# Optimization experiments

Measured on AMD Instinct MI355X. Metric: run time of the kernel, lower is better.

The kernel has to match this reference:

```python
import math
import jax, jax.numpy as jnp
import numpy as np

B, N, D, E, DN, H, M = 32, 64, 256, 32, 64, 8, 32
EPS = 1e-5


def _ln(x):
    # param-free layer norm over the last axis
    mu = jnp.mean(x, axis=-1, keepdims=True)
    var = jnp.var(x, axis=-1, keepdims=True)
    return (x - mu) * jax.lax.rsqrt(var + EPS)


def setup_inputs() -> dict:
    key = jax.random.key(0)
    ks = jax.random.split(key, 9)
    embeddings = jax.random.normal(ks[0], (B, N, D), dtype=jnp.float32)
    edge_features = jax.random.normal(ks[1], (B, N, N, E), dtype=jnp.float32)
    mask = jax.random.randint(ks[2], (B, N), 0, 2).astype(bool)
    node_features = jax.random.normal(ks[3], (B, N, DN), dtype=jnp.float32)
    s = lambda d: 1.0 / math.sqrt(d)
    W_edge = jax.random.normal(ks[4], (E, H, M), dtype=jnp.float32) * s(E)
    W_recv = jax.random.normal(ks[5], (D, H, M), dtype=jnp.float32) * s(D)
    W_send = jax.random.normal(ks[6], (D, H, M), dtype=jnp.float32) * s(D)
    W_recv_node = jax.random.normal(ks[7], (DN, H, M), dtype=jnp.float32) * s(DN)
    W_send_node = jax.random.normal(ks[8], (DN, H, M), dtype=jnp.float32) * s(DN)
    return dict(embeddings=embeddings, edge_features=edge_features, mask=mask,
                node_features=node_features, W_edge=W_edge, W_recv=W_recv,
                W_send=W_send, W_recv_node=W_recv_node, W_send_node=W_send_node)


def reference(embeddings, edge_features, mask, node_features,
              W_edge, W_recv, W_send, W_recv_node, W_send_node):
    sqrt2 = math.sqrt(2.0)
    mask_f = mask.astype(embeddings.dtype)  # [B, N]
    emb = _ln(embeddings) * mask_f[..., None]  # [B, N, D]
    # double mask: [B, sender, receiver, 1]
    dm = (mask_f[..., None, :, None] * mask_f[..., :, None, None])
    ef = edge_features * dm  # [B, N, N, E]
    # projections to (heads, message_dim)
    edge_part = jnp.einsum('bije,ehm->bijhm', ef, W_edge)        # [B,N,N,H,M]
    recv = jnp.einsum('bjd,dhm->bjhm', emb, W_recv) / sqrt2      # [B,N,H,M]
    send = jnp.einsum('bid,dhm->bihm', emb, W_send) / sqrt2
    # receiver broadcast over sender axis (-4), sender over receiver axis (-3)
    rs = jnp.tanh(recv[..., None, :, :, :] + send[..., :, None, :, :])  # [B,N,N,H,M]
    rn = jnp.einsum('bjd,dhm->bjhm', node_features, W_recv_node)
    sn = jnp.einsum('bid,dhm->bihm', node_features, W_send_node)
    rs = rs * jax.nn.sigmoid((rn[..., None, :, :, :] + sn[..., :, None, :, :]) / sqrt2)
    msgs = rs * edge_part * dm[..., None]  # [B,N,N,H,M]
    updates = msgs.sum(axis=-4)            # sum over senders -> [B,N,H,M]
    updates = _ln(updates)
    return jnp.reshape(updates, (*updates.shape[:-2], -1))  # [B,N,H*M]
```

## Files before the change

kernel.cpp:

```cpp
#include <hip/hip_runtime.h>
#include <hip/hip_bf16.h>
#include <math.h>

#define B_   32
#define N_   64
#define D_   256
#define E_   32
#define DN_  64
#define H_   8
#define M_   32
#define HM_  256
#define BN_  2048
#define EPS_ 1e-5f
#define INV_SQRT2 0.70710678118654752f

typedef float f32x4 __attribute__((ext_vector_type(4)));
typedef short bf16x8 __attribute__((ext_vector_type(8)));
union U4S8 { uint4 u; bf16x8 s; };

__device__ __forceinline__ unsigned pk2(float a, float b) {
    union { __hip_bfloat162 h; unsigned u; } cv;
    cv.h = __float22bfloat162_rn(make_float2(a, b));
    return cv.u;
}


__global__ __launch_bounds__(256, 1) void node_k(
        const float* __restrict__ emb, const float* __restrict__ nfeat,
        const int* __restrict__ mraw,
        const float* __restrict__ Wr, const float* __restrict__ Ws,
        const float* __restrict__ Wrn, const float* __restrict__ Wsn,
        float2* __restrict__ g_rr, float2* __restrict__ g_ssC,
        int* __restrict__ cnt, int* __restrict__ sidx,
        unsigned long long* __restrict__ mask64) {
    const int t = threadIdx.x;
    const int w = t >> 6, l = t & 63, hi = l >> 4, lo = l & 15;
    const int b = blockIdx.x >> 1, half = blockIdx.x & 1;
    const int nbase = half * 128 + w * 32;

    __shared__ int s_flag, cnt_sh;
    __shared__ float mfb[N_];
    __shared__ int sidx_s[N_], pos_s[N_];
    __shared__ __align__(16) unsigned short eln[64 * 256];
    __shared__ __align__(16) unsigned short nfs[64 * 64];

    if (t == 0) s_flag = 0;
    __syncthreads();
    {
        int v0 = mraw[t], v1 = mraw[t + 256];
        if (((v0 | v1) & ~1) != 0) atomicOr(&s_flag, 1);
    }
    __syncthreads();
    const bool bytef = (s_flag != 0);
    if (t < N_) {
        const unsigned char* mb = (const unsigned char*)mraw;
        const int k = b * N_ + t;
        mfb[t] = bytef ? (mb[k] ? 1.0f : 0.0f) : (mraw[k] ? 1.0f : 0.0f);
    }
    __syncthreads();
    if (t == 0) {
        int c = 0; unsigned long long bits = 0;
        for (int i = 0; i < N_; ++i) {
            if (mfb[i] > 0.5f) { bits |= (1ull << i); sidx_s[c] = i; pos_s[i] = c; ++c; }
            else pos_s[i] = -1;
        }
        cnt_sh = c;
        for (int p = c; p < N_; ++p) sidx_s[p] = -1;
        if (half == 0) { cnt[b] = c; mask64[b] = bits; }
    }
    __syncthreads();
    if (half == 0 && t < N_) sidx[b * N_ + t] = sidx_s[t];

    for (int rr = 0; rr < 16; ++rr) {
        const int i = w * 16 + rr;
        float4 x = *(const float4*)(emb + (size_t)(b * N_ + i) * D_ + l * 4);
        float s  = x.x + x.y + x.z + x.w;
        float s2 = x.x*x.x + x.y*x.y + x.z*x.z + x.w*x.w;
        #pragma unroll
        for (int k = 32; k >= 1; k >>= 1) { s += __shfl_xor(s, k); s2 += __shfl_xor(s2, k); }
        float mu  = s * (1.0f / D_);
        float var = s2 * (1.0f / D_) - mu * mu;
        float rs  = rsqrtf(var + EPS_) * mfb[i];
        unsigned p0 = pk2((x.x - mu) * rs, (x.y - mu) * rs);
        unsigned p1 = pk2((x.z - mu) * rs, (x.w - mu) * rs);
        unsigned off = (unsigned)(i * 512) + (((unsigned)(l * 8)) ^ (((unsigned)(i & 15)) << 4));
        *(uint2*)((char*)eln + off) = make_uint2(p0, p1);
    }
    #pragma unroll
    for (int it = 0; it < 4; ++it) {
        const int idx = it * 1024 + t * 4;
        const int r = idx >> 6, c = idx & 63;
        float4 x = *(const float4*)(nfeat + (size_t)(b * N_ + r) * DN_ + c);
        unsigned p0 = pk2(x.x, x.y), p1 = pk2(x.z, x.w);
        unsigned off = (unsigned)(r * 128) + (((unsigned)(c * 2)) ^ (((unsigned)(r & 7)) << 4));
        *(uint2*)((char*)nfs + off) = make_uint2(p0, p1);
    }
    __syncthreads();

    f32x4 aR[4][2], aS[4][2], aRN[4][2], aSN[4][2];
    #pragma unroll
    for (int mt = 0; mt < 4; ++mt)
        #pragma unroll
        for (int nt = 0; nt < 2; ++nt) {
            aR[mt][nt] = (f32x4){0,0,0,0}; aS[mt][nt] = (f32x4){0,0,0,0};
            aRN[mt][nt] = (f32x4){0,0,0,0}; aSN[mt][nt] = (f32x4){0,0,0,0};
        }

    for (int ks = 0; ks < 8; ++ks) {
        U4S8 af[4];
        #pragma unroll
        for (int mt = 0; mt < 4; ++mt) {
            const int i = mt * 16 + lo;
            unsigned o = (unsigned)(ks * 64 + hi * 16);
            af[mt].u = *(const uint4*)((const char*)eln +
                          (unsigned)(i * 512) + (o ^ (((unsigned)(i & 15)) << 4)));
        }
        U4S8 br[2], bs[2];
        #pragma unroll
        for (int nt = 0; nt < 2; ++nt) {
            const int n = nbase + nt * 16 + lo;
            const float* wr = Wr + (size_t)(ks * 32 + hi * 8) * HM_ + n;
            const float* ws = Ws + (size_t)(ks * 32 + hi * 8) * HM_ + n;
            float r0=wr[0*HM_], r1=wr[1*HM_], r2=wr[2*HM_], r3=wr[3*HM_];
            float r4=wr[4*HM_], r5=wr[5*HM_], r6=wr[6*HM_], r7=wr[7*HM_];
            br[nt].u = make_uint4(pk2(r0,r1), pk2(r2,r3), pk2(r4,r5), pk2(r6,r7));
            float s0=ws[0*HM_], s1=ws[1*HM_], s2=ws[2*HM_], s3=ws[3*HM_];
            float s4=ws[4*HM_], s5=ws[5*HM_], s6=ws[6*HM_], s7=ws[7*HM_];
            bs[nt].u = make_uint4(pk2(s0,s1), pk2(s2,s3), pk2(s4,s5), pk2(s6,s7));
        }
        #pragma unroll
        for (int mt = 0; mt < 4; ++mt)
            #pragma unroll
            for (int nt = 0; nt < 2; ++nt) {
                aR[mt][nt] = __builtin_amdgcn_mfma_f32_16x16x32_bf16(af[mt].s, br[nt].s, aR[mt][nt], 0, 0, 0);
                aS[mt][nt] = __builtin_amdgcn_mfma_f32_16x16x32_bf16(af[mt].s, bs[nt].s, aS[mt][nt], 0, 0, 0);
            }
        if (ks < 2) {
            U4S8 a2[4];
            #pragma unroll
            for (int mt = 0; mt < 4; ++mt) {
                const int i = mt * 16 + lo;
                unsigned o = (unsigned)(ks * 64 + hi * 16);
                a2[mt].u = *(const uint4*)((const char*)nfs +
                              (unsigned)(i * 128) + (o ^ (((unsigned)(i & 7)) << 4)));
            }
            U4S8 brn[2], bsn[2];
            #pragma unroll
            for (int nt = 0; nt < 2; ++nt) {
                const int n = nbase + nt * 16 + lo;
                const float* wr = Wrn + (size_t)(ks * 32 + hi * 8) * HM_ + n;
                const float* ws = Wsn + (size_t)(ks * 32 + hi * 8) * HM_ + n;
                float r0=wr[0*HM_], r1=wr[1*HM_], r2=wr[2*HM_], r3=wr[3*HM_];
                float r4=wr[4*HM_], r5=wr[5*HM_], r6=wr[6*HM_], r7=wr[7*HM_];
                brn[nt].u = make_uint4(pk2(r0,r1), pk2(r2,r3), pk2(r4,r5), pk2(r6,r7));
                float s0=ws[0*HM_], s1=ws[1*HM_], s2=ws[2*HM_], s3=ws[3*HM_];
                float s4=ws[4*HM_], s5=ws[5*HM_], s6=ws[6*HM_], s7=ws[7*HM_];
                bsn[nt].u = make_uint4(pk2(s0,s1), pk2(s2,s3), pk2(s4,s5), pk2(s6,s7));
            }
            #pragma unroll
            for (int mt = 0; mt < 4; ++mt)
                #pragma unroll
                for (int nt = 0; nt < 2; ++nt) {
                    aRN[mt][nt] = __builtin_amdgcn_mfma_f32_16x16x32_bf16(a2[mt].s, brn[nt].s, aRN[mt][nt], 0, 0, 0);
                    aSN[mt][nt] = __builtin_amdgcn_mfma_f32_16x16x32_bf16(a2[mt].s, bsn[nt].s, aSN[mt][nt], 0, 0, 0);
                }
        }
    }

    const int cb = cnt_sh;
    #pragma unroll
    for (int mt = 0; mt < 4; ++mt) {
        #pragma unroll
        for (int r = 0; r < 4; ++r) {
            const int i = mt * 16 + hi * 4 + r;
            const int p = pos_s[i];
            #pragma unroll
            for (int nt = 0; nt < 2; ++nt) {
                const int n = nbase + nt * 16 + lo;
                g_rr[(size_t)(b * N_ + i) * HM_ + n] =
                    make_float2(aR[mt][nt][r] * INV_SQRT2, aRN[mt][nt][r] * INV_SQRT2);
                if (p >= 0)
                    g_ssC[(size_t)(b * N_ + p) * HM_ + n] =
                        make_float2(aS[mt][nt][r] * INV_SQRT2, aSN[mt][nt][r] * INV_SQRT2);
            }
        }
    }
    for (int pp = cb + w; pp < N_; pp += 4) {
        float4 z = {0, 0, 0, 0};
        *(float4*)&g_ssC[(size_t)(b * N_ + pp) * HM_ + half * 128 + l * 2] = z;
    }
}

__global__ __launch_bounds__(256) void edge_agg(
        const float* __restrict__ edge,
        const unsigned long long* __restrict__ mask64,
        const int* __restrict__ cnt, const int* __restrict__ sidx,
        const float* __restrict__ We,
        const float2* __restrict__ g_rr, const float2* __restrict__ g_ssC,
        float* __restrict__ out) {
    const int t  = threadIdx.x;
    const int bn = blockIdx.x;
    const int b  = bn >> 6;
    const int j  = bn & 63;
    const int w  = t >> 6, l = t & 63, hi = l >> 4, lo = l & 15;

    if (!((mask64[b] >> j) & 1ull)) {
        out[bn * HM_ + t] = 0.0f;
        return;
    }
    const int cb = cnt[b];

    __shared__ uint4 ldsA[256];
    {
        const int mt = t >> 6, phi = (t >> 4) & 3, plo = t & 15;
        const int si = sidx[b * N_ + mt * 16 + plo];
        uint4 u = make_uint4(0, 0, 0, 0);
        if (si >= 0) {
            const float* src = edge + ((size_t)((b * N_ + si) * N_ + j)) * E_ + phi * 8;
            float4 v0 = *(const float4*)src;
            float4 v1 = *(const float4*)(src + 4);
            u = make_uint4(pk2(v0.x, v0.y), pk2(v0.z, v0.w),
                           pk2(v1.x, v1.y), pk2(v1.z, v1.w));
        }
        ldsA[t] = u;
    }
    __syncthreads();

    U4S8 b4[4];
    #pragma unroll
    for (int nl = 0; nl < 4; ++nl) {
        const int n = w * 64 + nl * 16 + lo;
        const float* wp = We + (size_t)(hi * 8) * HM_ + n;
        float w0=wp[0*HM_], w1=wp[1*HM_], w2=wp[2*HM_], w3=wp[3*HM_];
        float w4=wp[4*HM_], w5=wp[5*HM_], w6=wp[6*HM_], w7=wp[7*HM_];
        b4[nl].u = make_uint4(pk2(w0,w1), pk2(w2,w3), pk2(w4,w5), pk2(w6,w7));
    }

    float2 rr[4];
    #pragma unroll
    for (int nl = 0; nl < 4; ++nl) rr[nl] = g_rr[bn * HM_ + w * 64 + nl * 16 + lo];

    const f32x4 zero = {0.0f, 0.0f, 0.0f, 0.0f};
    float upd[4] = {0.0f, 0.0f, 0.0f, 0.0f};

    #pragma unroll
    for (int mt = 0; mt < 4; ++mt) {
        if (mt * 16 < cb) {
            U4S8 a4; a4.u = ldsA[mt * 64 + l];
            f32x4 acc[4];
            #pragma unroll
            for (int nl = 0; nl < 4; ++nl)
                acc[nl] = __builtin_amdgcn_mfma_f32_16x16x32_bf16(a4.s, b4[nl].s, zero, 0, 0, 0);

            #pragma unroll
            for (int r = 0; r < 4; ++r) {
                const int p = mt * 16 + hi * 4 + r;
                const float2* ssrow = g_ssC + (size_t)(b * N_ + p) * HM_;
                #pragma unroll
                for (int nl = 0; nl < 4; ++nl) {
                    float2 ss = ssrow[w * 64 + nl * 16 + lo];
                    float ep = acc[nl][r];
                    float tx = rr[nl].x + ss.x;
                    float E1 = __expf(2.0f * tx);
                    float th = fmaf(-2.0f, __builtin_amdgcn_rcpf(E1 + 1.0f), 1.0f);
                    float z  = rr[nl].y + ss.y;
                    float sg = __builtin_amdgcn_rcpf(1.0f + __expf(-z));
                    upd[nl] = fmaf(th * sg, ep, upd[nl]);
                }
            }
        }
    }

    #pragma unroll
    for (int nl = 0; nl < 4; ++nl) {
        upd[nl] += __shfl_xor(upd[nl], 16);
        upd[nl] += __shfl_xor(upd[nl], 32);
    }

    float s0 = upd[0] + upd[1], q0 = upd[0]*upd[0] + upd[1]*upd[1];
    float s1 = upd[2] + upd[3], q1 = upd[2]*upd[2] + upd[3]*upd[3];
    #pragma unroll
    for (int k = 8; k >= 1; k >>= 1) {
        s0 += __shfl_xor(s0, k); q0 += __shfl_xor(q0, k);
        s1 += __shfl_xor(s1, k); q1 += __shfl_xor(q1, k);
    }
    float mu0 = s0 * (1.0f / M_), va0 = q0 * (1.0f / M_) - mu0 * mu0;
    float mu1 = s1 * (1.0f / M_), va1 = q1 * (1.0f / M_) - mu1 * mu1;
    float rs0 = rsqrtf(va0 + EPS_), rs1 = rsqrtf(va1 + EPS_);
    float val = upd[hi];
    float o = (hi < 2) ? (val - mu0) * rs0 : (val - mu1) * rs1;
    out[bn * HM_ + w * 64 + l] = o;
}

extern "C" void kernel_launch(void* const* d_in, const int* in_sizes, int n_in,
                              void* d_out, int out_size, void* d_ws, size_t ws_size,
                              hipStream_t stream) {
    const float* embeddings = (const float*)d_in[0];
    const float* edge_feat  = (const float*)d_in[1];
    const int*   mask_raw   = (const int*)d_in[2];
    const float* node_feat  = (const float*)d_in[3];
    const float* W_edge     = (const float*)d_in[4];
    const float* W_recv     = (const float*)d_in[5];
    const float* W_send     = (const float*)d_in[6];
    const float* W_recvn    = (const float*)d_in[7];
    const float* W_sendn    = (const float*)d_in[8];
    float* out = (float*)d_out;

    float2* g_ssC = (float2*)d_ws;
    float2* g_rr  = g_ssC + (size_t)BN_ * HM_;
    unsigned long long* mask64 = (unsigned long long*)(g_rr + (size_t)BN_ * HM_);
    int* cnt  = (int*)(mask64 + B_);
    int* sidx = cnt + B_;

    node_k<<<2 * B_, 256, 0, stream>>>(embeddings, node_feat, mask_raw,
                                       W_recv, W_send, W_recvn, W_sendn,
                                       g_rr, g_ssC, cnt, sidx, mask64);
    edge_agg<<<BN_, 256, 0, stream>>>(edge_feat, mask64, cnt, sidx, W_edge,
                                      g_rr, g_ssC, out);
}
```

Before: 42.69 us.

## Fuse node projection and edge aggregation into one cooperative kernel with grid syncs

Replaces the two launches (64-block node projection, 2048-block edge aggregation) with a single 512-block cooperative kernel that uses grid.sync between three phases: layer norm/bf16 staging to global, a projection spread over all blocks, and edge aggregation with four receivers per block. It also folds tanh*sigmoid into one rational expression of two exps by pre-scaling the stored projections. The intent is to remove launch overhead and the poorly parallel 64-block projection phase; the cost is grid-wide barriers, an extra global round trip for normalized activations, and fewer, heavier aggregation blocks.

```diff
diff --git a/kernel.cpp b/kernel.cpp
--- a/kernel.cpp
+++ b/kernel.cpp
@@ -1,6 +1,9 @@
 #include <hip/hip_runtime.h>
 #include <hip/hip_bf16.h>
+#include <hip/hip_cooperative_groups.h>
 #include <math.h>
+
+namespace cg = cooperative_groups;
 
 #define B_   32
 #define N_   64
@@ -12,7 +15,8 @@
 #define HM_  256
 #define BN_  2048
 #define EPS_ 1e-5f
-#define INV_SQRT2 0.70710678118654752f
+#define SQRT2_    1.41421356237309515f
+#define NINVSQ2_ (-0.70710678118654752f)
 
 typedef float f32x4 __attribute__((ext_vector_type(4)));
 typedef short bf16x8 __attribute__((ext_vector_type(8)));
@@ -25,24 +29,24 @@
 }
 
 
-__global__ __launch_bounds__(256, 1) void node_k(
-        const float* __restrict__ emb, const float* __restrict__ nfeat,
-        const int* __restrict__ mraw,
-        const float* __restrict__ Wr, const float* __restrict__ Ws,
-        const float* __restrict__ Wrn, const float* __restrict__ Wsn,
+__global__ __launch_bounds__(256, 2) void fused_k(
+        const float* __restrict__ emb, const float* __restrict__ edge,
+        const int* __restrict__ mraw, const float* __restrict__ nfeat,
+        const float* __restrict__ We, const float* __restrict__ Wr,
+        const float* __restrict__ Ws, const float* __restrict__ Wrn,
+        const float* __restrict__ Wsn, float* __restrict__ out,
         float2* __restrict__ g_rr, float2* __restrict__ g_ssC,
-        int* __restrict__ cnt, int* __restrict__ sidx,
-        unsigned long long* __restrict__ mask64) {
+        unsigned short* __restrict__ eln, unsigned short* __restrict__ nfs,
+        int* __restrict__ cnt, int* __restrict__ sidx, int* __restrict__ pos,
+        unsigned long long* __restrict__ mask64)
+{
+    cg::grid_group grid = cg::this_grid();
+    const int blk = blockIdx.x;
     const int t = threadIdx.x;
     const int w = t >> 6, l = t & 63, hi = l >> 4, lo = l & 15;
-    const int b = blockIdx.x >> 1, half = blockIdx.x & 1;
-    const int nbase = half * 128 + w * 32;
-
-    __shared__ int s_flag, cnt_sh;
-    __shared__ float mfb[N_];
-    __shared__ int sidx_s[N_], pos_s[N_];
-    __shared__ __align__(16) unsigned short eln[64 * 256];
-    __shared__ __align__(16) unsigned short nfs[64 * 64];
+
+    __shared__ int s_flag;
+    __shared__ __align__(16) uint4 ldsA[4][256];
 
     if (t == 0) s_flag = 0;
     __syncthreads();
@@ -52,244 +56,180 @@
     }
     __syncthreads();
     const bool bytef = (s_flag != 0);
-    if (t < N_) {
-        const unsigned char* mb = (const unsigned char*)mraw;
-        const int k = b * N_ + t;
-        mfb[t] = bytef ? (mb[k] ? 1.0f : 0.0f) : (mraw[k] ? 1.0f : 0.0f);
-    }
-    __syncthreads();
-    if (t == 0) {
-        int c = 0; unsigned long long bits = 0;
-        for (int i = 0; i < N_; ++i) {
-            if (mfb[i] > 0.5f) { bits |= (1ull << i); sidx_s[c] = i; pos_s[i] = c; ++c; }
-            else pos_s[i] = -1;
-        }
-        cnt_sh = c;
-        for (int p = c; p < N_; ++p) sidx_s[p] = -1;
-        if (half == 0) { cnt[b] = c; mask64[b] = bits; }
-    }
-    __syncthreads();
-    if (half == 0 && t < N_) sidx[b * N_ + t] = sidx_s[t];
-
-    for (int rr = 0; rr < 16; ++rr) {
-        const int i = w * 16 + rr;
-        float4 x = *(const float4*)(emb + (size_t)(b * N_ + i) * D_ + l * 4);
+    const unsigned char* mbb = (const unsigned char*)mraw;
+
+    {
+        const int bn = blk * 4 + w;
+        const float mfv = (bytef ? (mbb[bn] != 0) : (mraw[bn] != 0)) ? 1.0f : 0.0f;
+        float4 x = *(const float4*)(emb + (size_t)bn * D_ + l * 4);
         float s  = x.x + x.y + x.z + x.w;
         float s2 = x.x*x.x + x.y*x.y + x.z*x.z + x.w*x.w;
         #pragma unroll
         for (int k = 32; k >= 1; k >>= 1) { s += __shfl_xor(s, k); s2 += __shfl_xor(s2, k); }
         float mu  = s * (1.0f / D_);
         float var = s2 * (1.0f / D_) - mu * mu;
-        float rs  = rsqrtf(var + EPS_) * mfb[i];
-        unsigned p0 = pk2((x.x - mu) * rs, (x.y - mu) * rs);
-        unsigned p1 = pk2((x.z - mu) * rs, (x.w - mu) * rs);
-        unsigned off = (unsigned)(i * 512) + (((unsigned)(l * 8)) ^ (((unsigned)(i & 15)) << 4));
-        *(uint2*)((char*)eln + off) = make_uint2(p0, p1);
-    }
-    #pragma unroll
-    for (int it = 0; it < 4; ++it) {
-        const int idx = it * 1024 + t * 4;
-        const int r = idx >> 6, c = idx & 63;
-        float4 x = *(const float4*)(nfeat + (size_t)(b * N_ + r) * DN_ + c);
-        unsigned p0 = pk2(x.x, x.y), p1 = pk2(x.z, x.w);
-        unsigned off = (unsigned)(r * 128) + (((unsigned)(c * 2)) ^ (((unsigned)(r & 7)) << 4));
-        *(uint2*)((char*)nfs + off) = make_uint2(p0, p1);
-    }
-    __syncthreads();
-
-    f32x4 aR[4][2], aS[4][2], aRN[4][2], aSN[4][2];
-    #pragma unroll
-    for (int mt = 0; mt < 4; ++mt)
-        #pragma unroll
-        for (int nt = 0; nt < 2; ++nt) {
-            aR[mt][nt] = (f32x4){0,0,0,0}; aS[mt][nt] = (f32x4){0,0,0,0};
-            aRN[mt][nt] = (f32x4){0,0,0,0}; aSN[mt][nt] = (f32x4){0,0,0,0};
-        }
-
-    for (int ks = 0; ks < 8; ++ks) {
-        U4S8 af[4];
-        #pragma unroll
-        for (int mt = 0; mt < 4; ++mt) {
-            const int i = mt * 16 + lo;
-            unsigned o = (unsigned)(ks * 64 + hi * 16);
-            af[mt].u = *(const uint4*)((const char*)eln +
-                          (unsigned)(i * 512) + (o ^ (((unsigned)(i & 15)) << 4)));
-        }
-        U4S8 br[2], bs[2];
-        #pragma unroll
-        for (int nt = 0; nt < 2; ++nt) {
-            const int n = nbase + nt * 16 + lo;
-            const float* wr = Wr + (size_t)(ks * 32 + hi * 8) * HM_ + n;
-            const float* ws = Ws + (size_t)(ks * 32 + hi * 8) * HM_ + n;
-            float r0=wr[0*HM_], r1=wr[1*HM_], r2=wr[2*HM_], r3=wr[3*HM_];
-            float r4=wr[4*HM_], r5=wr[5*HM_], r6=wr[6*HM_], r7=wr[7*HM_];
-            br[nt].u = make_uint4(pk2(r0,r1), pk2(r2,r3), pk2(r4,r5), pk2(r6,r7));
-            float s0=ws[0*HM_], s1=ws[1*HM_], s2=ws[2*HM_], s3=ws[3*HM_];
-            float s4=ws[4*HM_], s5=ws[5*HM_], s6=ws[6*HM_], s7=ws[7*HM_];
-            bs[nt].u = make_uint4(pk2(s0,s1), pk2(s2,s3), pk2(s4,s5), pk2(s6,s7));
-        }
-        #pragma unroll
-        for (int mt = 0; mt < 4; ++mt)
-            #pragma unroll
-            for (int nt = 0; nt < 2; ++nt) {
-                aR[mt][nt] = __builtin_amdgcn_mfma_f32_16x16x32_bf16(af[mt].s, br[nt].s, aR[mt][nt], 0, 0, 0);
-                aS[mt][nt] = __builtin_amdgcn_mfma_f32_16x16x32_bf16(af[mt].s, bs[nt].s, aS[mt][nt], 0, 0, 0);
+        float rs  = rsqrtf(var + EPS_) * mfv;
+        *(uint2*)(eln + (size_t)bn * D_ + l * 4) =
+            make_uint2(pk2((x.x - mu) * rs, (x.y - mu) * rs),
+                       pk2((x.z - mu) * rs, (x.w - mu) * rs));
+        if (l < 32) {
+            float2 f2 = *(const float2*)(nfeat + (size_t)bn * DN_ + l * 2);
+            *(unsigned*)(nfs + (size_t)bn * DN_ + l * 2) = pk2(f2.x, f2.y);
+        }
+    }
+    if (blk < B_ && t == 0) {
+        int c = 0; unsigned long long bits = 0;
+        for (int i = 0; i < N_; ++i) {
+            const int k = blk * N_ + i;
+            const bool on = bytef ? (mbb[k] != 0) : (mraw[k] != 0);
+            if (on) { bits |= (1ull << i); sidx[blk * N_ + c] = i; pos[k] = c; ++c; }
+            else pos[k] = -1;
+        }
+        cnt[blk] = c; mask64[blk] = bits;
+        for (int p = c; p < N_; ++p) sidx[blk * N_ + p] = -1;
+    }
+
+    grid.sync();
+
+    {
+        const int b2 = blk >> 4, chunk = blk & 15;
+        const int nb = chunk * 16 + lo;
+        const int mt2 = w;
+        const size_t arow = (size_t)(b2 * N_ + mt2 * 16 + lo);
+
+        f32x4 aR = {0,0,0,0}, aS = {0,0,0,0}, aRN = {0,0,0,0}, aSN = {0,0,0,0};
+        #pragma unroll
+        for (int ks = 0; ks < 8; ++ks) {
+            U4S8 a; a.u = *(const uint4*)(eln + arow * D_ + ks * 32 + hi * 8);
+            const float* wrp = Wr + (size_t)(ks * 32 + hi * 8) * HM_ + nb;
+            const float* wsp = Ws + (size_t)(ks * 32 + hi * 8) * HM_ + nb;
+            U4S8 br, bs;
+            br.u = make_uint4(pk2(wrp[0],      wrp[HM_]),     pk2(wrp[2*HM_], wrp[3*HM_]),
+                              pk2(wrp[4*HM_],  wrp[5*HM_]),   pk2(wrp[6*HM_], wrp[7*HM_]));
+            bs.u = make_uint4(pk2(wsp[0],      wsp[HM_]),     pk2(wsp[2*HM_], wsp[3*HM_]),
+                              pk2(wsp[4*HM_],  wsp[5*HM_]),   pk2(wsp[6*HM_], wsp[7*HM_]));
+            aR = __builtin_amdgcn_mfma_f32_16x16x32_bf16(a.s, br.s, aR, 0, 0, 0);
+            aS = __builtin_amdgcn_mfma_f32_16x16x32_bf16(a.s, bs.s, aS, 0, 0, 0);
+            if (ks < 2) {
+                U4S8 a2; a2.u = *(const uint4*)(nfs + arow * DN_ + ks * 32 + hi * 8);
+                const float* wrn = Wrn + (size_t)(ks * 32 + hi * 8) * HM_ + nb;
+                const float* wsn = Wsn + (size_t)(ks * 32 + hi * 8) * HM_ + nb;
+                U4S8 brn, bsn;
+                brn.u = make_uint4(pk2(wrn[0],     wrn[HM_]),   pk2(wrn[2*HM_], wrn[3*HM_]),
+                                   pk2(wrn[4*HM_], wrn[5*HM_]), pk2(wrn[6*HM_], wrn[7*HM_]));
+                bsn.u = make_uint4(pk2(wsn[0],     wsn[HM_]),   pk2(wsn[2*HM_], wsn[3*HM_]),
+                                   pk2(wsn[4*HM_], wsn[5*HM_]), pk2(wsn[6*HM_], wsn[7*HM_]));
+                aRN = __builtin_amdgcn_mfma_f32_16x16x32_bf16(a2.s, brn.s, aRN, 0, 0, 0);
+                aSN = __builtin_amdgcn_mfma_f32_16x16x32_bf16(a2.s, bsn.s, aSN, 0, 0, 0);
             }
-        if (ks < 2) {
-            U4S8 a2[4];
-            #pragma unroll
-            for (int mt = 0; mt < 4; ++mt) {
-                const int i = mt * 16 + lo;
-                unsigned o = (unsigned)(ks * 64 + hi * 16);
-                a2[mt].u = *(const uint4*)((const char*)nfs +
-                              (unsigned)(i * 128) + (o ^ (((unsigned)(i & 7)) << 4)));
-            }
-            U4S8 brn[2], bsn[2];
-            #pragma unroll
-            for (int nt = 0; nt < 2; ++nt) {
-                const int n = nbase + nt * 16 + lo;
-                const float* wr = Wrn + (size_t)(ks * 32 + hi * 8) * HM_ + n;
-                const float* ws = Wsn + (size_t)(ks * 32 + hi * 8) * HM_ + n;
-                float r0=wr[0*HM_], r1=wr[1*HM_], r2=wr[2*HM_], r3=wr[3*HM_];
-                float r4=wr[4*HM_], r5=wr[5*HM_], r6=wr[6*HM_], r7=wr[7*HM_];
-                brn[nt].u = make_uint4(pk2(r0,r1), pk2(r2,r3), pk2(r4,r5), pk2(r6,r7));
-                float s0=ws[0*HM_], s1=ws[1*HM_], s2=ws[2*HM_], s3=ws[3*HM_];
-                float s4=ws[4*HM_], s5=ws[5*HM_], s6=ws[6*HM_], s7=ws[7*HM_];
-                bsn[nt].u = make_uint4(pk2(s0,s1), pk2(s2,s3), pk2(s4,s5), pk2(s6,s7));
-            }
-            #pragma unroll
-            for (int mt = 0; mt < 4; ++mt)
-                #pragma unroll
-                for (int nt = 0; nt < 2; ++nt) {
-                    aRN[mt][nt] = __builtin_amdgcn_mfma_f32_16x16x32_bf16(a2[mt].s, brn[nt].s, aRN[mt][nt], 0, 0, 0);
-                    aSN[mt][nt] = __builtin_amdgcn_mfma_f32_16x16x32_bf16(a2[mt].s, bsn[nt].s, aSN[mt][nt], 0, 0, 0);
-                }
-        }
-    }
-
-    const int cb = cnt_sh;
-    #pragma unroll
-    for (int mt = 0; mt < 4; ++mt) {
+        }
+        const int cb2 = cnt[b2];
         #pragma unroll
         for (int r = 0; r < 4; ++r) {
-            const int i = mt * 16 + hi * 4 + r;
-            const int p = pos_s[i];
-            #pragma unroll
-            for (int nt = 0; nt < 2; ++nt) {
-                const int n = nbase + nt * 16 + lo;
-                g_rr[(size_t)(b * N_ + i) * HM_ + n] =
-                    make_float2(aR[mt][nt][r] * INV_SQRT2, aRN[mt][nt][r] * INV_SQRT2);
-                if (p >= 0)
-                    g_ssC[(size_t)(b * N_ + p) * HM_ + n] =
-                        make_float2(aS[mt][nt][r] * INV_SQRT2, aSN[mt][nt][r] * INV_SQRT2);
-            }
-        }
-    }
-    for (int pp = cb + w; pp < N_; pp += 4) {
-        float4 z = {0, 0, 0, 0};
-        *(float4*)&g_ssC[(size_t)(b * N_ + pp) * HM_ + half * 128 + l * 2] = z;
-    }
-}
-
-__global__ __launch_bounds__(256) void edge_agg(
-        const float* __restrict__ edge,
-        const unsigned long long* __restrict__ mask64,
-        const int* __restrict__ cnt, const int* __restrict__ sidx,
-        const float* __restrict__ We,
-        const float2* __restrict__ g_rr, const float2* __restrict__ g_ssC,
-        float* __restrict__ out) {
-    const int t  = threadIdx.x;
-    const int bn = blockIdx.x;
-    const int b  = bn >> 6;
-    const int j  = bn & 63;
-    const int w  = t >> 6, l = t & 63, hi = l >> 4, lo = l & 15;
-
-    if (!((mask64[b] >> j) & 1ull)) {
-        out[bn * HM_ + t] = 0.0f;
-        return;
-    }
+            const int i = mt2 * 16 + hi * 4 + r;
+            g_rr[(size_t)(b2 * N_ + i) * HM_ + nb] =
+                make_float2(SQRT2_ * aR[r], NINVSQ2_ * aRN[r]);
+            const int p = pos[b2 * N_ + i];
+            if (p >= 0)
+                g_ssC[(size_t)(b2 * N_ + p) * HM_ + nb] =
+                    make_float2(SQRT2_ * aS[r], NINVSQ2_ * aSN[r]);
+        }
+        for (int p = cb2 + (t >> 4); p < N_; p += 16)
+            g_ssC[(size_t)(b2 * N_ + p) * HM_ + chunk * 16 + (t & 15)] = make_float2(0.f, 0.f);
+    }
+
+    grid.sync();
+
+    const int b  = blk >> 4;
+    const int j0 = (blk & 15) * 4;
+    const unsigned long long mbits = mask64[b];
     const int cb = cnt[b];
 
-    __shared__ uint4 ldsA[256];
     {
         const int mt = t >> 6, phi = (t >> 4) & 3, plo = t & 15;
         const int si = sidx[b * N_ + mt * 16 + plo];
-        uint4 u = make_uint4(0, 0, 0, 0);
         if (si >= 0) {
-            const float* src = edge + ((size_t)((b * N_ + si) * N_ + j)) * E_ + phi * 8;
-            float4 v0 = *(const float4*)src;
-            float4 v1 = *(const float4*)(src + 4);
-            u = make_uint4(pk2(v0.x, v0.y), pk2(v0.z, v0.w),
-                           pk2(v1.x, v1.y), pk2(v1.z, v1.w));
-        }
-        ldsA[t] = u;
+            const float* rb = edge + ((size_t)((b * N_ + si) * N_ + j0)) * E_ + phi * 8;
+            #pragma unroll
+            for (int q = 0; q < 4; ++q) {
+                float4 v0 = *(const float4*)(rb + q * E_);
+                float4 v1 = *(const float4*)(rb + q * E_ + 4);
+                ldsA[q][t] = make_uint4(pk2(v0.x, v0.y), pk2(v0.z, v0.w),
+                                        pk2(v1.x, v1.y), pk2(v1.z, v1.w));
+            }
+        } else {
+            #pragma unroll
+            for (int q = 0; q < 4; ++q) ldsA[q][t] = make_uint4(0, 0, 0, 0);
+        }
     }
     __syncthreads();
 
     U4S8 b4[4];
     #pragma unroll
     for (int nl = 0; nl < 4; ++nl) {
-        const int n = w * 64 + nl * 16 + lo;
-        const float* wp = We + (size_t)(hi * 8) * HM_ + n;
-        float w0=wp[0*HM_], w1=wp[1*HM_], w2=wp[2*HM_], w3=wp[3*HM_];
-        float w4=wp[4*HM_], w5=wp[5*HM_], w6=wp[6*HM_], w7=wp[7*HM_];
-        b4[nl].u = make_uint4(pk2(w0,w1), pk2(w2,w3), pk2(w4,w5), pk2(w6,w7));
-    }
-
-    float2 rr[4];
+        const float* wp = We + (size_t)(hi * 8) * HM_ + w * 64 + nl * 16 + lo;
+        b4[nl].u = make_uint4(pk2(wp[0],      wp[HM_]),     pk2(wp[2*HM_], wp[3*HM_]),
+                              pk2(wp[4*HM_],  wp[5*HM_]),   pk2(wp[6*HM_], wp[7*HM_]));
+    }
+
+    const f32x4 zero = {0.0f, 0.0f, 0.0f, 0.0f};
     #pragma unroll
-    for (int nl = 0; nl < 4; ++nl) rr[nl] = g_rr[bn * HM_ + w * 64 + nl * 16 + lo];
-
-    const f32x4 zero = {0.0f, 0.0f, 0.0f, 0.0f};
-    float upd[4] = {0.0f, 0.0f, 0.0f, 0.0f};
-
-    #pragma unroll
-    for (int mt = 0; mt < 4; ++mt) {
-        if (mt * 16 < cb) {
-            U4S8 a4; a4.u = ldsA[mt * 64 + l];
-            f32x4 acc[4];
-            #pragma unroll
-            for (int nl = 0; nl < 4; ++nl)
-                acc[nl] = __builtin_amdgcn_mfma_f32_16x16x32_bf16(a4.s, b4[nl].s, zero, 0, 0, 0);
-
-            #pragma unroll
-            for (int r = 0; r < 4; ++r) {
-                const int p = mt * 16 + hi * 4 + r;
-                const float2* ssrow = g_ssC + (size_t)(b * N_ + p) * HM_;
+    for (int q = 0; q < 4; ++q) {
+        const int j = j0 + q, bn = b * N_ + j;
+        if (!((mbits >> j) & 1ull)) {
+            out[(size_t)bn * HM_ + w * 64 + l] = 0.0f;
+            continue;
+        }
+        float2 rr[4];
+        #pragma unroll
+        for (int nl = 0; nl < 4; ++nl) rr[nl] = g_rr[(size_t)bn * HM_ + w * 64 + nl * 16 + lo];
+
+        float upd[4] = {0.0f, 0.0f, 0.0f, 0.0f};
+        #pragma unroll
+        for (int mt = 0; mt < 4; ++mt) {
+            if (mt * 16 < cb) {
+                U4S8 a; a.u = ldsA[q][mt * 64 + l];
+                f32x4 acc[4];
                 #pragma unroll
-                for (int nl = 0; nl < 4; ++nl) {
-                    float2 ss = ssrow[w * 64 + nl * 16 + lo];
-                    float ep = acc[nl][r];
-                    float tx = rr[nl].x + ss.x;
-                    float E1 = __expf(2.0f * tx);
-                    float th = fmaf(-2.0f, __builtin_amdgcn_rcpf(E1 + 1.0f), 1.0f);
-                    float z  = rr[nl].y + ss.y;
-                    float sg = __builtin_amdgcn_rcpf(1.0f + __expf(-z));
-                    upd[nl] = fmaf(th * sg, ep, upd[nl]);
+                for (int nl = 0; nl < 4; ++nl)
+                    acc[nl] = __builtin_amdgcn_mfma_f32_16x16x32_bf16(a.s, b4[nl].s, zero, 0, 0, 0);
+                #pragma unroll
+                for (int r = 0; r < 4; ++r) {
+                    const float2* ssrow =
+                        g_ssC + (size_t)(b * N_ + mt * 16 + hi * 4 + r) * HM_ + w * 64 + lo;
+                    #pragma unroll
+                    for (int nl = 0; nl < 4; ++nl) {
+                        float2 ss = ssrow[nl * 16];
+                        float u = __expf(rr[nl].x + ss.x);
+                        float v = __expf(rr[nl].y + ss.y);
+                        float den = (u + 1.0f) * (1.0f + v);
+                        float g = (u - 1.0f) * __builtin_amdgcn_rcpf(den);
+                        upd[nl] = fmaf(g, acc[nl][r], upd[nl]);
+                    }
                 }
             }
         }
-    }
-
-    #pragma unroll
-    for (int nl = 0; nl < 4; ++nl) {
-        upd[nl] += __shfl_xor(upd[nl], 16);
-        upd[nl] += __shfl_xor(upd[nl], 32);
-    }
-
-    float s0 = upd[0] + upd[1], q0 = upd[0]*upd[0] + upd[1]*upd[1];
-    float s1 = upd[2] + upd[3], q1 = upd[2]*upd[2] + upd[3]*upd[3];
-    #pragma unroll
-    for (int k = 8; k >= 1; k >>= 1) {
-        s0 += __shfl_xor(s0, k); q0 += __shfl_xor(q0, k);
-        s1 += __shfl_xor(s1, k); q1 += __shfl_xor(q1, k);
-    }
-    float mu0 = s0 * (1.0f / M_), va0 = q0 * (1.0f / M_) - mu0 * mu0;
-    float mu1 = s1 * (1.0f / M_), va1 = q1 * (1.0f / M_) - mu1 * mu1;
-    float rs0 = rsqrtf(va0 + EPS_), rs1 = rsqrtf(va1 + EPS_);
-    float val = upd[hi];
-    float o = (hi < 2) ? (val - mu0) * rs0 : (val - mu1) * rs1;
-    out[bn * HM_ + w * 64 + l] = o;
+        #pragma unroll
+        for (int nl = 0; nl < 4; ++nl) {
+            upd[nl] += __shfl_xor(upd[nl], 16);
+            upd[nl] += __shfl_xor(upd[nl], 32);
+        }
+        float s0 = upd[0] + upd[1], q0 = upd[0]*upd[0] + upd[1]*upd[1];
+        float s1 = upd[2] + upd[3], q1 = upd[2]*upd[2] + upd[3]*upd[3];
+        #pragma unroll
+        for (int k = 8; k >= 1; k >>= 1) {
+            s0 += __shfl_xor(s0, k); q0 += __shfl_xor(q0, k);
+            s1 += __shfl_xor(s1, k); q1 += __shfl_xor(q1, k);
+        }
+        float mu0 = s0 * (1.0f / M_), va0 = q0 * (1.0f / M_) - mu0 * mu0;
+        float mu1 = s1 * (1.0f / M_), va1 = q1 * (1.0f / M_) - mu1 * mu1;
+        float rs0 = rsqrtf(va0 + EPS_), rs1 = rsqrtf(va1 + EPS_);
+        float v01 = (hi & 1) ? upd[1] : upd[0];
+        float v23 = (hi & 1) ? upd[3] : upd[2];
+        float val = (hi < 2) ? v01 : v23;
+        float o = (hi < 2) ? (val - mu0) * rs0 : (val - mu1) * rs1;
+        out[(size_t)bn * HM_ + w * 64 + l] = o;
+    }
 }
 
 extern "C" void kernel_launch(void* const* d_in, const int* in_sizes, int n_in,
@@ -308,13 +248,19 @@
 
     float2* g_ssC = (float2*)d_ws;
     float2* g_rr  = g_ssC + (size_t)BN_ * HM_;
-    unsigned long long* mask64 = (unsigned long long*)(g_rr + (size_t)BN_ * HM_);
+    unsigned short* eln = (unsigned short*)(g_rr + (size_t)BN_ * HM_);
+    unsigned short* nfs = eln + (size_t)BN_ * D_;
+    unsigned long long* mask64 = (unsigned long long*)(nfs + (size_t)BN_ * DN_);
     int* cnt  = (int*)(mask64 + B_);
     int* sidx = cnt + B_;
-
-    node_k<<<2 * B_, 256, 0, stream>>>(embeddings, node_feat, mask_raw,
-                                       W_recv, W_send, W_recvn, W_sendn,
-                                       g_rr, g_ssC, cnt, sidx, mask64);
-    edge_agg<<<BN_, 256, 0, stream>>>(edge_feat, mask64, cnt, sidx, W_edge,
-                                      g_rr, g_ssC, out);
+    int* pos  = sidx + BN_;
+
+    void* args[] = { (void*)&embeddings, (void*)&edge_feat, (void*)&mask_raw,
+                     (void*)&node_feat, (void*)&W_edge, (void*)&W_recv,
+                     (void*)&W_send, (void*)&W_recvn, (void*)&W_sendn,
+                     (void*)&out, (void*)&g_rr, (void*)&g_ssC,
+                     (void*)&eln, (void*)&nfs, (void*)&cnt, (void*)&sidx,
+                     (void*)&pos, (void*)&mask64 };
+    (void)hipLaunchCooperativeKernel((const void*)fused_k, dim3(512), dim3(256),
+                                     args, 0, stream);
 }
```

Measured after the change: 145.9 us. +241.8%, slower.

## Precompute exponentials per node and fuse tanh-sigmoid into one reciprocal; batch receivers per block

Applied to the files above, without the earlier changes.

The node kernel now stores exp(sqrt2*r) and exp(-r/sqrt2) factors instead of raw projections. This lets the edge kernel compute tanh(a+b)*sigmoid(c+d) as (uv-1)/((uv+1)(pq+1)), using products and a single reciprocal with no per-edge exp calls. The edge kernel also handles four receivers per block so the W_edge fragments and sender ssC values are loaded into registers once and reused, and node_k is split into four column chunks per batch for more blocks. The cost is higher register pressure from the 64-entry ssv array, plus a risk of overflow or inf in the exp products when activations are large.

```diff
diff --git a/kernel.cpp b/kernel.cpp
--- a/kernel.cpp
+++ b/kernel.cpp
@@ -12,7 +12,8 @@
 #define HM_  256
 #define BN_  2048
 #define EPS_ 1e-5f
-#define INV_SQRT2 0.70710678118654752f
+#define SQRT2_    1.41421356237309515f
+#define NINVSQ2_ (-0.70710678118654752f)
 
 typedef float f32x4 __attribute__((ext_vector_type(4)));
 typedef short bf16x8 __attribute__((ext_vector_type(8)));
@@ -25,7 +26,7 @@
 }
 
 
-__global__ __launch_bounds__(256, 1) void node_k(
+__global__ __launch_bounds__(256, 2) void node_k(
         const float* __restrict__ emb, const float* __restrict__ nfeat,
         const int* __restrict__ mraw,
         const float* __restrict__ Wr, const float* __restrict__ Ws,
@@ -35,8 +36,7 @@
         unsigned long long* __restrict__ mask64) {
     const int t = threadIdx.x;
     const int w = t >> 6, l = t & 63, hi = l >> 4, lo = l & 15;
-    const int b = blockIdx.x >> 1, half = blockIdx.x & 1;
-    const int nbase = half * 128 + w * 32;
+    const int b = blockIdx.x >> 2, c = blockIdx.x & 3;
 
     __shared__ int s_flag, cnt_sh;
     __shared__ float mfb[N_];
@@ -52,24 +52,24 @@
     }
     __syncthreads();
     const bool bytef = (s_flag != 0);
+    const unsigned char* mbb = (const unsigned char*)mraw;
     if (t < N_) {
-        const unsigned char* mb = (const unsigned char*)mraw;
         const int k = b * N_ + t;
-        mfb[t] = bytef ? (mb[k] ? 1.0f : 0.0f) : (mraw[k] ? 1.0f : 0.0f);
+        mfb[t] = (bytef ? (mbb[k] != 0) : (mraw[k] != 0)) ? 1.0f : 0.0f;
     }
     __syncthreads();
     if (t == 0) {
-        int c = 0; unsigned long long bits = 0;
+        int cc = 0; unsigned long long bits = 0;
         for (int i = 0; i < N_; ++i) {
-            if (mfb[i] > 0.5f) { bits |= (1ull << i); sidx_s[c] = i; pos_s[i] = c; ++c; }
+            if (mfb[i] > 0.5f) { bits |= (1ull << i); sidx_s[cc] = i; pos_s[i] = cc; ++cc; }
             else pos_s[i] = -1;
         }
-        cnt_sh = c;
-        for (int p = c; p < N_; ++p) sidx_s[p] = -1;
-        if (half == 0) { cnt[b] = c; mask64[b] = bits; }
-    }
-    __syncthreads();
-    if (half == 0 && t < N_) sidx[b * N_ + t] = sidx_s[t];
+        cnt_sh = cc;
+        for (int p = cc; p < N_; ++p) sidx_s[p] = -1;
+        if (c == 0) { cnt[b] = cc; mask64[b] = bits; }
+    }
+    __syncthreads();
+    if (c == 0 && t < N_) sidx[b * N_ + t] = sidx_s[t];
 
     for (int rr = 0; rr < 16; ++rr) {
         const int i = w * 16 + rr;
@@ -89,81 +89,55 @@
     #pragma unroll
     for (int it = 0; it < 4; ++it) {
         const int idx = it * 1024 + t * 4;
-        const int r = idx >> 6, c = idx & 63;
-        float4 x = *(const float4*)(nfeat + (size_t)(b * N_ + r) * DN_ + c);
-        unsigned p0 = pk2(x.x, x.y), p1 = pk2(x.z, x.w);
-        unsigned off = (unsigned)(r * 128) + (((unsigned)(c * 2)) ^ (((unsigned)(r & 7)) << 4));
-        *(uint2*)((char*)nfs + off) = make_uint2(p0, p1);
-    }
-    __syncthreads();
-
-    f32x4 aR[4][2], aS[4][2], aRN[4][2], aSN[4][2];
-    #pragma unroll
-    for (int mt = 0; mt < 4; ++mt)
-        #pragma unroll
-        for (int nt = 0; nt < 2; ++nt) {
-            aR[mt][nt] = (f32x4){0,0,0,0}; aS[mt][nt] = (f32x4){0,0,0,0};
-            aRN[mt][nt] = (f32x4){0,0,0,0}; aSN[mt][nt] = (f32x4){0,0,0,0};
-        }
-
+        const int r = idx >> 6, cc = idx & 63;
+        float4 x = *(const float4*)(nfeat + (size_t)(b * N_ + r) * DN_ + cc);
+        unsigned off = (unsigned)(r * 128) + (((unsigned)(cc * 2)) ^ (((unsigned)(r & 7)) << 4));
+        *(uint2*)((char*)nfs + off) = make_uint2(pk2(x.x, x.y), pk2(x.z, x.w));
+    }
+    __syncthreads();
+
+    const int nb = c * 64 + w * 16 + lo;
+    f32x4 aR[4], aS[4], aRN[4], aSN[4];
+    #pragma unroll
+    for (int mt = 0; mt < 4; ++mt) {
+        aR[mt] = (f32x4){0,0,0,0}; aS[mt] = (f32x4){0,0,0,0};
+        aRN[mt] = (f32x4){0,0,0,0}; aSN[mt] = (f32x4){0,0,0,0};
+    }
+    #pragma unroll
     for (int ks = 0; ks < 8; ++ks) {
-        U4S8 af[4];
+        const float* wrp = Wr + (size_t)(ks * 32 + hi * 8) * HM_ + nb;
+        const float* wsp = Ws + (size_t)(ks * 32 + hi * 8) * HM_ + nb;
+        U4S8 br, bs;
+        br.u = make_uint4(pk2(wrp[0],     wrp[HM_]),    pk2(wrp[2*HM_], wrp[3*HM_]),
+                          pk2(wrp[4*HM_], wrp[5*HM_]),  pk2(wrp[6*HM_], wrp[7*HM_]));
+        bs.u = make_uint4(pk2(wsp[0],     wsp[HM_]),    pk2(wsp[2*HM_], wsp[3*HM_]),
+                          pk2(wsp[4*HM_], wsp[5*HM_]),  pk2(wsp[6*HM_], wsp[7*HM_]));
         #pragma unroll
         for (int mt = 0; mt < 4; ++mt) {
             const int i = mt * 16 + lo;
             unsigned o = (unsigned)(ks * 64 + hi * 16);
-            af[mt].u = *(const uint4*)((const char*)eln +
+            U4S8 a; a.u = *(const uint4*)((const char*)eln +
                           (unsigned)(i * 512) + (o ^ (((unsigned)(i & 15)) << 4)));
-        }
-        U4S8 br[2], bs[2];
-        #pragma unroll
-        for (int nt = 0; nt < 2; ++nt) {
-            const int n = nbase + nt * 16 + lo;
-            const float* wr = Wr + (size_t)(ks * 32 + hi * 8) * HM_ + n;
-            const float* ws = Ws + (size_t)(ks * 32 + hi * 8) * HM_ + n;
-            float r0=wr[0*HM_], r1=wr[1*HM_], r2=wr[2*HM_], r3=wr[3*HM_];
-            float r4=wr[4*HM_], r5=wr[5*HM_], r6=wr[6*HM_], r7=wr[7*HM_];
-            br[nt].u = make_uint4(pk2(r0,r1), pk2(r2,r3), pk2(r4,r5), pk2(r6,r7));
-            float s0=ws[0*HM_], s1=ws[1*HM_], s2=ws[2*HM_], s3=ws[3*HM_];
-            float s4=ws[4*HM_], s5=ws[5*HM_], s6=ws[6*HM_], s7=ws[7*HM_];
-            bs[nt].u = make_uint4(pk2(s0,s1), pk2(s2,s3), pk2(s4,s5), pk2(s6,s7));
-        }
-        #pragma unroll
-        for (int mt = 0; mt < 4; ++mt)
-            #pragma unroll
-            for (int nt = 0; nt < 2; ++nt) {
-                aR[mt][nt] = __builtin_amdgcn_mfma_f32_16x16x32_bf16(af[mt].s, br[nt].s, aR[mt][nt], 0, 0, 0);
-                aS[mt][nt] = __builtin_amdgcn_mfma_f32_16x16x32_bf16(af[mt].s, bs[nt].s, aS[mt][nt], 0, 0, 0);
-            }
+            aR[mt] = __builtin_amdgcn_mfma_f32_16x16x32_bf16(a.s, br.s, aR[mt], 0, 0, 0);
+            aS[mt] = __builtin_amdgcn_mfma_f32_16x16x32_bf16(a.s, bs.s, aS[mt], 0, 0, 0);
+        }
         if (ks < 2) {
-            U4S8 a2[4];
+            const float* wrn = Wrn + (size_t)(ks * 32 + hi * 8) * HM_ + nb;
+            const float* wsn = Wsn + (size_t)(ks * 32 + hi * 8) * HM_ + nb;
+            U4S8 brn, bsn;
+            brn.u = make_uint4(pk2(wrn[0],     wrn[HM_]),   pk2(wrn[2*HM_], wrn[3*HM_]),
+                               pk2(wrn[4*HM_], wrn[5*HM_]), pk2(wrn[6*HM_], wrn[7*HM_]));
+            bsn.u = make_uint4(pk2(wsn[0],     wsn[HM_]),   pk2(wsn[2*HM_], wsn[3*HM_]),
+                               pk2(wsn[4*HM_], wsn[5*HM_]), pk2(wsn[6*HM_], wsn[7*HM_]));
             #pragma unroll
             for (int mt = 0; mt < 4; ++mt) {
                 const int i = mt * 16 + lo;
                 unsigned o = (unsigned)(ks * 64 + hi * 16);
-                a2[mt].u = *(const uint4*)((const char*)nfs +
+                U4S8 a2; a2.u = *(const uint4*)((const char*)nfs +
                               (unsigned)(i * 128) + (o ^ (((unsigned)(i & 7)) << 4)));
+                aRN[mt] = __builtin_amdgcn_mfma_f32_16x16x32_bf16(a2.s, brn.s, aRN[mt], 0, 0, 0);
+                aSN[mt] = __builtin_amdgcn_mfma_f32_16x16x32_bf16(a2.s, bsn.s, aSN[mt], 0, 0, 0);
             }
-            U4S8 brn[2], bsn[2];
-            #pragma unroll
-            for (int nt = 0; nt < 2; ++nt) {
-                const int n = nbase + nt * 16 + lo;
-                const float* wr = Wrn + (size_t)(ks * 32 + hi * 8) * HM_ + n;
-                const float* ws = Wsn + (size_t)(ks * 32 + hi * 8) * HM_ + n;
-                float r0=wr[0*HM_], r1=wr[1*HM_], r2=wr[2*HM_], r3=wr[3*HM_];
-                float r4=wr[4*HM_], r5=wr[5*HM_], r6=wr[6*HM_], r7=wr[7*HM_];
-                brn[nt].u = make_uint4(pk2(r0,r1), pk2(r2,r3), pk2(r4,r5), pk2(r6,r7));
-                float s0=ws[0*HM_], s1=ws[1*HM_], s2=ws[2*HM_], s3=ws[3*HM_];
-                float s4=ws[4*HM_], s5=ws[5*HM_], s6=ws[6*HM_], s7=ws[7*HM_];
-                bsn[nt].u = make_uint4(pk2(s0,s1), pk2(s2,s3), pk2(s4,s5), pk2(s6,s7));
-            }
-            #pragma unroll
-            for (int mt = 0; mt < 4; ++mt)
-                #pragma unroll
-                for (int nt = 0; nt < 2; ++nt) {
-                    aRN[mt][nt] = __builtin_amdgcn_mfma_f32_16x16x32_bf16(a2[mt].s, brn[nt].s, aRN[mt][nt], 0, 0, 0);
-                    aSN[mt][nt] = __builtin_amdgcn_mfma_f32_16x16x32_bf16(a2[mt].s, bsn[nt].s, aSN[mt][nt], 0, 0, 0);
-                }
         }
     }
 
@@ -173,123 +147,137 @@
         #pragma unroll
         for (int r = 0; r < 4; ++r) {
             const int i = mt * 16 + hi * 4 + r;
+            float U = __expf(SQRT2_  * aR[mt][r]);
+            float P = __expf(NINVSQ2_ * aRN[mt][r]);
+            g_rr[(size_t)(b * N_ + i) * HM_ + nb] = make_float2(U, P);
             const int p = pos_s[i];
-            #pragma unroll
-            for (int nt = 0; nt < 2; ++nt) {
-                const int n = nbase + nt * 16 + lo;
-                g_rr[(size_t)(b * N_ + i) * HM_ + n] =
-                    make_float2(aR[mt][nt][r] * INV_SQRT2, aRN[mt][nt][r] * INV_SQRT2);
-                if (p >= 0)
-                    g_ssC[(size_t)(b * N_ + p) * HM_ + n] =
-                        make_float2(aS[mt][nt][r] * INV_SQRT2, aSN[mt][nt][r] * INV_SQRT2);
+            if (p >= 0) {
+                float V = __expf(SQRT2_  * aS[mt][r]);
+                float Q = __expf(NINVSQ2_ * aSN[mt][r]);
+                g_ssC[(size_t)(b * N_ + p) * HM_ + nb] = make_float2(V, Q);
             }
         }
     }
-    for (int pp = cb + w; pp < N_; pp += 4) {
-        float4 z = {0, 0, 0, 0};
-        *(float4*)&g_ssC[(size_t)(b * N_ + pp) * HM_ + half * 128 + l * 2] = z;
-    }
+    for (int p = cb + w; p < N_; p += 4)
+        g_ssC[(size_t)(b * N_ + p) * HM_ + c * 64 + l] = make_float2(0.f, 0.f);
 }
 
-__global__ __launch_bounds__(256) void edge_agg(
-        const float* __restrict__ edge,
+__global__ __launch_bounds__(256, 2) void edge_k(
+        const float* __restrict__ edge, const float* __restrict__ We,
+        const float2* __restrict__ g_rr, const float2* __restrict__ g_ssC,
         const unsigned long long* __restrict__ mask64,
         const int* __restrict__ cnt, const int* __restrict__ sidx,
-        const float* __restrict__ We,
-        const float2* __restrict__ g_rr, const float2* __restrict__ g_ssC,
         float* __restrict__ out) {
-    const int t  = threadIdx.x;
-    const int bn = blockIdx.x;
-    const int b  = bn >> 6;
-    const int j  = bn & 63;
-    const int w  = t >> 6, l = t & 63, hi = l >> 4, lo = l & 15;
-
-    if (!((mask64[b] >> j) & 1ull)) {
-        out[bn * HM_ + t] = 0.0f;
+    const int t = threadIdx.x;
+    const int w = t >> 6, l = t & 63, hi = l >> 4, lo = l & 15;
+    const int blk = blockIdx.x;
+    const int b = blk >> 4, j0 = (blk & 15) * 4;
+    const unsigned long long mbits = mask64[b];
+    const int cb = cnt[b];
+
+    if (((mbits >> j0) & 15ull) == 0ull) {
+        #pragma unroll
+        for (int q = 0; q < 4; ++q)
+            out[(size_t)(b * N_ + j0 + q) * HM_ + t] = 0.0f;
         return;
     }
-    const int cb = cnt[b];
-
-    __shared__ uint4 ldsA[256];
+
+    __shared__ __align__(16) uint4 ldsA[4][256];
+
     {
         const int mt = t >> 6, phi = (t >> 4) & 3, plo = t & 15;
         const int si = sidx[b * N_ + mt * 16 + plo];
-        uint4 u = make_uint4(0, 0, 0, 0);
         if (si >= 0) {
-            const float* src = edge + ((size_t)((b * N_ + si) * N_ + j)) * E_ + phi * 8;
-            float4 v0 = *(const float4*)src;
-            float4 v1 = *(const float4*)(src + 4);
-            u = make_uint4(pk2(v0.x, v0.y), pk2(v0.z, v0.w),
-                           pk2(v1.x, v1.y), pk2(v1.z, v1.w));
-        }
-        ldsA[t] = u;
-    }
-    __syncthreads();
+            const float* rb = edge + ((size_t)((b * N_ + si) * N_ + j0)) * E_ + phi * 8;
+            #pragma unroll
+            for (int q = 0; q < 4; ++q) {
+                float4 v0 = *(const float4*)(rb + q * E_);
+                float4 v1 = *(const float4*)(rb + q * E_ + 4);
+                ldsA[q][t] = make_uint4(pk2(v0.x, v0.y), pk2(v0.z, v0.w),
+                                        pk2(v1.x, v1.y), pk2(v1.z, v1.w));
+            }
+        } else {
+            #pragma unroll
+            for (int q = 0; q < 4; ++q) ldsA[q][t] = make_uint4(0, 0, 0, 0);
+        }
+    }
+
+    float2 ssv[4][4][4];
+    #pragma unroll
+    for (int mt = 0; mt < 4; ++mt)
+        #pragma unroll
+        for (int r = 0; r < 4; ++r) {
+            const float2* srow = g_ssC + (size_t)(b * N_ + mt * 16 + hi * 4 + r) * HM_
+                                       + w * 64 + lo;
+            #pragma unroll
+            for (int nl = 0; nl < 4; ++nl) ssv[mt][r][nl] = srow[nl * 16];
+        }
 
     U4S8 b4[4];
     #pragma unroll
     for (int nl = 0; nl < 4; ++nl) {
-        const int n = w * 64 + nl * 16 + lo;
-        const float* wp = We + (size_t)(hi * 8) * HM_ + n;
-        float w0=wp[0*HM_], w1=wp[1*HM_], w2=wp[2*HM_], w3=wp[3*HM_];
-        float w4=wp[4*HM_], w5=wp[5*HM_], w6=wp[6*HM_], w7=wp[7*HM_];
-        b4[nl].u = make_uint4(pk2(w0,w1), pk2(w2,w3), pk2(w4,w5), pk2(w6,w7));
-    }
-
-    float2 rr[4];
-    #pragma unroll
-    for (int nl = 0; nl < 4; ++nl) rr[nl] = g_rr[bn * HM_ + w * 64 + nl * 16 + lo];
+        const float* wp = We + (size_t)(hi * 8) * HM_ + w * 64 + nl * 16 + lo;
+        b4[nl].u = make_uint4(pk2(wp[0],     wp[HM_]),    pk2(wp[2*HM_], wp[3*HM_]),
+                              pk2(wp[4*HM_], wp[5*HM_]),  pk2(wp[6*HM_], wp[7*HM_]));
+    }
+    __syncthreads();
 
     const f32x4 zero = {0.0f, 0.0f, 0.0f, 0.0f};
-    float upd[4] = {0.0f, 0.0f, 0.0f, 0.0f};
-
-    #pragma unroll
-    for (int mt = 0; mt < 4; ++mt) {
-        if (mt * 16 < cb) {
-            U4S8 a4; a4.u = ldsA[mt * 64 + l];
-            f32x4 acc[4];
-            #pragma unroll
-            for (int nl = 0; nl < 4; ++nl)
-                acc[nl] = __builtin_amdgcn_mfma_f32_16x16x32_bf16(a4.s, b4[nl].s, zero, 0, 0, 0);
-
-            #pragma unroll
-            for (int r = 0; r < 4; ++r) {
-                const int p = mt * 16 + hi * 4 + r;
-                const float2* ssrow = g_ssC + (size_t)(b * N_ + p) * HM_;
+    #pragma unroll
+    for (int q = 0; q < 4; ++q) {
+        const int j = j0 + q, bn = b * N_ + j;
+        if (!((mbits >> j) & 1ull)) {
+            out[(size_t)bn * HM_ + w * 64 + l] = 0.0f;
+            continue;
+        }
+        float2 rrv[4];
+        #pragma unroll
+        for (int nl = 0; nl < 4; ++nl)
+            rrv[nl] = g_rr[(size_t)bn * HM_ + w * 64 + nl * 16 + lo];
+
+        float upd[4] = {0.0f, 0.0f, 0.0f, 0.0f};
+        #pragma unroll
+        for (int mt = 0; mt < 4; ++mt) {
+            if (mt * 16 < cb) {
+                U4S8 a; a.u = ldsA[q][mt * 64 + l];
+                f32x4 acc[4];
                 #pragma unroll
-                for (int nl = 0; nl < 4; ++nl) {
-                    float2 ss = ssrow[w * 64 + nl * 16 + lo];
-                    float ep = acc[nl][r];
-                    float tx = rr[nl].x + ss.x;
-                    float E1 = __expf(2.0f * tx);
-                    float th = fmaf(-2.0f, __builtin_amdgcn_rcpf(E1 + 1.0f), 1.0f);
-                    float z  = rr[nl].y + ss.y;
-                    float sg = __builtin_amdgcn_rcpf(1.0f + __expf(-z));
-                    upd[nl] = fmaf(th * sg, ep, upd[nl]);
+                for (int nl = 0; nl < 4; ++nl)
+                    acc[nl] = __builtin_amdgcn_mfma_f32_16x16x32_bf16(a.s, b4[nl].s, zero, 0, 0, 0);
+                #pragma unroll
+                for (int r = 0; r < 4; ++r) {
+                    #pragma unroll
+                    for (int nl = 0; nl < 4; ++nl) {
+                        float u = rrv[nl].x * ssv[mt][r][nl].x;
+                        float v = rrv[nl].y * ssv[mt][r][nl].y;
+                        float den = (u + 1.0f) * (v + 1.0f);
+                        float g = (u - 1.0f) * __builtin_amdgcn_rcpf(den);
+                        upd[nl] = fmaf(g, acc[nl][r], upd[nl]);
+                    }
                 }
             }
         }
-    }
-
-    #pragma unroll
-    for (int nl = 0; nl < 4; ++nl) {
-        upd[nl] += __shfl_xor(upd[nl], 16);
-        upd[nl] += __shfl_xor(upd[nl], 32);
-    }
-
-    float s0 = upd[0] + upd[1], q0 = upd[0]*upd[0] + upd[1]*upd[1];
-    float s1 = upd[2] + upd[3], q1 = upd[2]*upd[2] + upd[3]*upd[3];
-    #pragma unroll
-    for (int k = 8; k >= 1; k >>= 1) {
-        s0 += __shfl_xor(s0, k); q0 += __shfl_xor(q0, k);
-        s1 += __shfl_xor(s1, k); q1 += __shfl_xor(q1, k);
-    }
-    float mu0 = s0 * (1.0f / M_), va0 = q0 * (1.0f / M_) - mu0 * mu0;
-    float mu1 = s1 * (1.0f / M_), va1 = q1 * (1.0f / M_) - mu1 * mu1;
-    float rs0 = rsqrtf(va0 + EPS_), rs1 = rsqrtf(va1 + EPS_);
-    float val = upd[hi];
-    float o = (hi < 2) ? (val - mu0) * rs0 : (val - mu1) * rs1;
-    out[bn * HM_ + w * 64 + l] = o;
+        #pragma unroll
+        for (int nl = 0; nl < 4; ++nl) {
+            upd[nl] += __shfl_xor(upd[nl], 16);
+            upd[nl] += __shfl_xor(upd[nl], 32);
+        }
+        float s0 = upd[0] + upd[1], q0 = upd[0]*upd[0] + upd[1]*upd[1];
+        float s1 = upd[2] + upd[3], q1 = upd[2]*upd[2] + upd[3]*upd[3];
+        #pragma unroll
+        for (int k = 8; k >= 1; k >>= 1) {
+            s0 += __shfl_xor(s0, k); q0 += __shfl_xor(q0, k);
+            s1 += __shfl_xor(s1, k); q1 += __shfl_xor(q1, k);
+        }
+        float mu0 = s0 * (1.0f / M_), va0 = q0 * (1.0f / M_) - mu0 * mu0;
+        float mu1 = s1 * (1.0f / M_), va1 = q1 * (1.0f / M_) - mu1 * mu1;
+        float rs0 = rsqrtf(va0 + EPS_), rs1 = rsqrtf(va1 + EPS_);
+        float v01 = (hi & 1) ? upd[1] : upd[0];
+        float v23 = (hi & 1) ? upd[3] : upd[2];
+        float val = (hi < 2) ? v01 : v23;
+        float o = (hi < 2) ? (val - mu0) * rs0 : (val - mu1) * rs1;
+        out[(size_t)bn * HM_ + w * 64 + l] = o;
+    }
 }
 
 extern "C" void kernel_launch(void* const* d_in, const int* in_sizes, int n_in,
@@ -312,9 +300,9 @@
     int* cnt  = (int*)(mask64 + B_);
     int* sidx = cnt + B_;
 
-    node_k<<<2 * B_, 256, 0, stream>>>(embeddings, node_feat, mask_raw,
+    node_k<<<4 * B_, 256, 0, stream>>>(embeddings, node_feat, mask_raw,
                                        W_recv, W_send, W_recvn, W_sendn,
                                        g_rr, g_ssC, cnt, sidx, mask64);
-    edge_agg<<<BN_, 256, 0, stream>>>(edge_feat, mask64, cnt, sidx, W_edge,
-                                      g_rr, g_ssC, out);
+    edge_k<<<BN_ / 4, 256, 0, stream>>>(edge_feat, W_edge, g_rr, g_ssC,
+                                        mask64, cnt, sidx, out);
 }
```

Measured after the change: 43.71 us. +2.4%, slower.
